# Kernel tuning notes

Hardware: AMD Instinct MI355X
Metric: run time of the kernel (lower is better)

The kernel has to match this reference:

```python
import jax, jax.numpy as jnp
import numpy as np

# (multiplicity, irrep_dim) for irreps_in == irreps_out: 128x0e + 64x1o + 32x2e
IRREPS = [(128, 1), (64, 3), (32, 5)]
NUM_INDICES = 64
N_ELEMENTS = 8192
SCALE = 1.0  # module's `scale` arg; total coeff = scale / sqrt(num_indices) / sqrt(mul_in)
W_DIM = sum(m * m for m, _ in IRREPS)  # 21504


def setup_inputs() -> dict:
    key = jax.random.key(0)
    ks = jax.random.split(key, 5)
    x0 = jax.random.normal(ks[0], (N_ELEMENTS, 128, 1), jnp.float32)
    x1 = jax.random.normal(ks[1], (N_ELEMENTS, 64, 3), jnp.float32)
    x2 = jax.random.normal(ks[2], (N_ELEMENTS, 32, 5), jnp.float32)
    w = jax.random.normal(ks[3], (NUM_INDICES, W_DIM), jnp.float32)
    # Random contiguous segment sizes that sum exactly to N_ELEMENTS:
    bnd = jnp.sort(jax.random.randint(ks[4], (NUM_INDICES - 1,), 0, N_ELEMENTS + 1)).astype(jnp.int32)
    counts = jnp.diff(jnp.concatenate([jnp.zeros((1,), jnp.int32), bnd,
                                       jnp.full((1,), N_ELEMENTS, jnp.int32)]))
    return {"x0": x0, "x1": x1, "x2": x2, "w": w, "num_index_counts": counts}


def reference(x0, x1, x2, w, num_index_counts):
    """Indexed (segmented) equivariant linear: rows are grouped contiguously by
    num_index_counts; segment g uses weight row w[g]. Per matched irrep the
    weight block is a (mul_in, mul_out) mixing matrix applied identically to
    each of the ir.dim components (Schur's lemma), with fan-in normalization
    1/sqrt(mul_in) (cue.descriptors.linear) times scale/sqrt(num_indices)."""
    n = x0.shape[0]
    # segment id per row (rows are already grouped contiguously, as in Repeats())
    sid = jnp.repeat(jnp.arange(NUM_INDICES), num_index_counts, total_repeat_length=n)
    xs = (x0, x1, x2)
    ys = []
    off = 0
    for xk, (mul, ir_dim) in zip(xs, IRREPS):
        blk = w[:, off:off + mul * mul].reshape(NUM_INDICES, mul, mul)  # (E, m_in, m_out)
        coeff = float(SCALE / np.sqrt(NUM_INDICES) / np.sqrt(mul))
        wk = blk[sid]  # (n, m_in, m_out) per-row weight gather
        # y[n, o, i] = coeff * sum_m x[n, m, i] * w[g(n), m, o]
        ys.append(coeff * jnp.einsum('nmi,nmo->noi', xk, wk))
        off += mul * mul
    return tuple(ys)
```

## Files before the change

### kernel.cpp

```cpp
#include <hip/hip_runtime.h>

typedef __attribute__((ext_vector_type(8))) short bf16x8;
typedef __attribute__((ext_vector_type(4))) float f32x4;

#define NSEG 64
#define NROW 8192
#define WROW 21504
#define NBPP 576
#define T0   64
#define T12  16
#define PA   136
#define PB   136
#define P1   196
#define P2   164

__device__ __forceinline__ unsigned short f2bf(float f) {
    unsigned u = __float_as_uint(f);
    u += 0x7fffu + ((u >> 16) & 1u);
    return (unsigned short)(u >> 16);
}

__global__ __launch_bounds__(256) void iil_kernel(
    const float* __restrict__ x0, const float* __restrict__ x1, const float* __restrict__ x2,
    const float* __restrict__ w, const int* __restrict__ counts,
    float* __restrict__ y0, float* __restrict__ y1, float* __restrict__ y2)
{
    __shared__ __align__(16) unsigned short smem_u[T0 * PA + 128 * PB];
    __shared__ int sstart[NSEG + 1];
    __shared__ int t16s[NSEG + 1];
    __shared__ int t64s[NSEG + 1];

    const int t = threadIdx.x;

    if (t < NSEG) {
        int c = counts[t];
        int v = c;
        #pragma unroll
        for (int d = 1; d < NSEG; d <<= 1) {
            int u = __shfl_up(v, d, 64);
            if (t >= d) v += u;
        }
        sstart[t + 1] = v;
        int a = (c + 15) >> 4;
        #pragma unroll
        for (int d = 1; d < NSEG; d <<= 1) {
            int u = __shfl_up(a, d, 64);
            if (t >= d) a += u;
        }
        t16s[t + 1] = a;
        int b2 = (c + 63) >> 6;
        #pragma unroll
        for (int d = 1; d < NSEG; d <<= 1) {
            int u = __shfl_up(b2, d, 64);
            if (t >= d) b2 += u;
        }
        t64s[t + 1] = b2;
        if (t == 0) { sstart[0] = 0; t16s[0] = 0; t64s[0] = 0; }
    }
    __syncthreads();

    const int phase = blockIdx.x / NBPP;
    const int pb = blockIdx.x - phase * NBPP;
    const float4 z4 = make_float4(0.f, 0.f, 0.f, 0.f);
    float* sbuf = (float*)smem_u;

    if (phase == 0) {
        if (pb >= t64s[NSEG]) return;
        int lo = 0, hi = NSEG;
        while (hi - lo > 1) {
            int mid = (lo + hi) >> 1;
            if (t64s[mid] <= pb) lo = mid; else hi = mid;
        }
        const int g = lo;
        const int s = sstart[g] + (pb - t64s[g]) * T0;
        const int nr = min(T0, sstart[g + 1] - s);
        const float* __restrict__ wseg = w + (size_t)g * WROW;

        unsigned short* As = smem_u;
        unsigned short* Bs = smem_u + T0 * PA;

        const float4* g0 = (const float4*)x0 + (size_t)s * 32;
        #pragma unroll
        for (int i = 0; i < 8; ++i) {
            int idx = t + i * 256;
            int r = idx >> 5, c4 = (idx & 31) * 4;
            float4 v = (r < nr) ? g0[idx] : z4;
            ushort4 bv;
            bv.x = f2bf(v.x); bv.y = f2bf(v.y); bv.z = f2bf(v.z); bv.w = f2bf(v.w);
            *(ushort4*)(As + r * PA + c4) = bv;
        }
        #pragma unroll
        for (int i = 0; i < 8; ++i) {
            int idx = t + i * 256;
            int k2 = idx >> 5;
            int o4 = (idx & 31) * 4;
            float4 va = *(const float4*)(wseg + (size_t)(2 * k2) * 128 + o4);
            float4 vb = *(const float4*)(wseg + (size_t)(2 * k2 + 1) * 128 + o4);
            *(ushort2*)(Bs + (size_t)(o4 + 0) * PB + 2 * k2) = make_ushort2(f2bf(va.x), f2bf(vb.x));
            *(ushort2*)(Bs + (size_t)(o4 + 1) * PB + 2 * k2) = make_ushort2(f2bf(va.y), f2bf(vb.y));
            *(ushort2*)(Bs + (size_t)(o4 + 2) * PB + 2 * k2) = make_ushort2(f2bf(va.z), f2bf(vb.z));
            *(ushort2*)(Bs + (size_t)(o4 + 3) * PB + 2 * k2) = make_ushort2(f2bf(va.w), f2bf(vb.w));
        }
        __syncthreads();

        const int lane = t & 63;
        const int wv = t >> 6;
        const int l16 = lane & 15;
        const int quad = lane >> 4;
        const int mp = wv & 1;
        const int np = wv >> 1;

        f32x4 acc[2][4];
        #pragma unroll
        for (int mt = 0; mt < 2; ++mt)
            #pragma unroll
            for (int nt = 0; nt < 4; ++nt)
                acc[mt][nt] = (f32x4){0.f, 0.f, 0.f, 0.f};

        const unsigned short* Abase = As + ((2 * mp) * 16 + l16) * PA + quad * 8;
        const unsigned short* Bbase = Bs + (size_t)((4 * np) * 16 + l16) * PB + quad * 8;

        #pragma unroll
        for (int ks = 0; ks < 4; ++ks) {
            const int ko = ks * 32;
            bf16x8 a0 = *(const bf16x8*)(Abase + ko);
            bf16x8 a1 = *(const bf16x8*)(Abase + 16 * PA + ko);
            #pragma unroll
            for (int nt = 0; nt < 4; ++nt) {
                bf16x8 b = *(const bf16x8*)(Bbase + (size_t)nt * 16 * PB + ko);
                acc[0][nt] = __builtin_amdgcn_mfma_f32_16x16x32_bf16(a0, b, acc[0][nt], 0, 0, 0);
                acc[1][nt] = __builtin_amdgcn_mfma_f32_16x16x32_bf16(a1, b, acc[1][nt], 0, 0, 0);
            }
        }

        const float c0 = 0.011048543456039806f;
        #pragma unroll
        for (int mt = 0; mt < 2; ++mt) {
            int rbase = (2 * mp + mt) * 16 + quad * 4;
            #pragma unroll
            for (int nt = 0; nt < 4; ++nt) {
                int col = (4 * np + nt) * 16 + l16;
                #pragma unroll
                for (int rg = 0; rg < 4; ++rg) {
                    int r = rbase + rg;
                    if (r < nr)
                        y0[(size_t)(s + r) * 128 + col] = acc[mt][nt][rg] * c0;
                }
            }
        }
    } else if (phase == 1) {
        if (pb >= t16s[NSEG]) return;
        int lo = 0, hi = NSEG;
        while (hi - lo > 1) {
            int mid = (lo + hi) >> 1;
            if (t16s[mid] <= pb) lo = mid; else hi = mid;
        }
        const int g = lo;
        const int s = sstart[g] + (pb - t16s[g]) * T12;
        const int nr = min(T12, sstart[g + 1] - s);
        const float* __restrict__ wseg = w + (size_t)g * WROW;

        float* sx1 = sbuf;
        const float4* g1 = (const float4*)x1 + (size_t)s * 48;
        #pragma unroll
        for (int i = 0; i < 3; ++i) {
            int idx = t + i * 256;
            int r = idx / 48, c = idx - r * 48;
            float4 v = (r < nr) ? g1[idx] : z4;
            *(float4*)(sx1 + r * P1 + c * 4) = v;
        }
        __syncthreads();

        const int og = t & 15;
        const int r = t >> 4;
        const float* xrow = sx1 + r * P1;
        const float* wp = wseg + 16384 + og * 4;
        float acc[12];
        #pragma unroll
        for (int i = 0; i < 12; ++i) acc[i] = 0.f;
        #pragma unroll 2
        for (int kq = 0; kq < 16; ++kq) {
            float4 xq0 = *(const float4*)(xrow + 12 * kq + 0);
            float4 xq1 = *(const float4*)(xrow + 12 * kq + 4);
            float4 xq2 = *(const float4*)(xrow + 12 * kq + 8);
            float xf[12] = {xq0.x, xq0.y, xq0.z, xq0.w,
                            xq1.x, xq1.y, xq1.z, xq1.w,
                            xq2.x, xq2.y, xq2.z, xq2.w};
            #pragma unroll
            for (int kk = 0; kk < 4; ++kk) {
                float4 wv = *(const float4*)(wp + (size_t)(4 * kq + kk) * 64);
                #pragma unroll
                for (int oo = 0; oo < 4; ++oo) {
                    float wvo = (oo == 0) ? wv.x : (oo == 1) ? wv.y : (oo == 2) ? wv.z : wv.w;
                    acc[oo * 3 + 0] = fmaf(wvo, xf[kk * 3 + 0], acc[oo * 3 + 0]);
                    acc[oo * 3 + 1] = fmaf(wvo, xf[kk * 3 + 1], acc[oo * 3 + 1]);
                    acc[oo * 3 + 2] = fmaf(wvo, xf[kk * 3 + 2], acc[oo * 3 + 2]);
                }
            }
        }
        const float c1 = 0.015625f;
        if (r < nr) {
            float* yb = y1 + (size_t)(s + r) * 192 + og * 12;
            *(float4*)(yb + 0) = make_float4(acc[0] * c1, acc[1] * c1, acc[2] * c1, acc[3] * c1);
            *(float4*)(yb + 4) = make_float4(acc[4] * c1, acc[5] * c1, acc[6] * c1, acc[7] * c1);
            *(float4*)(yb + 8) = make_float4(acc[8] * c1, acc[9] * c1, acc[10] * c1, acc[11] * c1);
        }
    } else {
        if (pb >= t16s[NSEG]) return;
        int lo = 0, hi = NSEG;
        while (hi - lo > 1) {
            int mid = (lo + hi) >> 1;
            if (t16s[mid] <= pb) lo = mid; else hi = mid;
        }
        const int g = lo;
        const int s = sstart[g] + (pb - t16s[g]) * T12;
        const int nr = min(T12, sstart[g + 1] - s);
        const float* __restrict__ wseg = w + (size_t)g * WROW;

        float* sx2 = sbuf;
        const float4* g2 = (const float4*)x2 + (size_t)s * 40;
        #pragma unroll
        for (int i = 0; i < 3; ++i) {
            int idx = t + i * 256;
            if (idx < 640) {
                int r = idx / 40, c = idx - r * 40;
                float4 v = (r < nr) ? g2[idx] : z4;
                *(float4*)(sx2 + r * P2 + c * 4) = v;
            }
        }
        __syncthreads();

        const int og = t & 15;
        const int r = t >> 4;
        const float* xrow = sx2 + r * P2;
        const float* wp = wseg + 20480 + og * 2;
        float acc[10];
        #pragma unroll
        for (int i = 0; i < 10; ++i) acc[i] = 0.f;
        #pragma unroll
        for (int kq = 0; kq < 8; ++kq) {
            float xf[20];
            #pragma unroll
            for (int j = 0; j < 5; ++j) {
                float4 v = *(const float4*)(xrow + 20 * kq + 4 * j);
                xf[4 * j + 0] = v.x; xf[4 * j + 1] = v.y; xf[4 * j + 2] = v.z; xf[4 * j + 3] = v.w;
            }
            #pragma unroll
            for (int kk = 0; kk < 4; ++kk) {
                float2 wv = *(const float2*)(wp + (size_t)(4 * kq + kk) * 32);
                #pragma unroll
                for (int i = 0; i < 5; ++i) {
                    acc[i]     = fmaf(wv.x, xf[5 * kk + i], acc[i]);
                    acc[5 + i] = fmaf(wv.y, xf[5 * kk + i], acc[5 + i]);
                }
            }
        }
        const float c2 = 0.022097086912079608f;
        if (r < nr) {
            float* yb = y2 + (size_t)(s + r) * 160 + og * 10;
            #pragma unroll
            for (int i = 0; i < 5; ++i)
                *(float2*)(yb + 2 * i) = make_float2(acc[2 * i] * c2, acc[2 * i + 1] * c2);
        }
    }
}

extern "C" void kernel_launch(void* const* d_in, const int* in_sizes, int n_in,
                              void* d_out, int out_size, void* d_ws, size_t ws_size,
                              hipStream_t stream) {
    const float* x0 = (const float*)d_in[0];
    const float* x1 = (const float*)d_in[1];
    const float* x2 = (const float*)d_in[2];
    const float* w  = (const float*)d_in[3];
    const int* counts = (const int*)d_in[4];

    float* y0 = (float*)d_out;
    float* y1 = y0 + (size_t)NROW * 128;
    float* y2 = y1 + (size_t)NROW * 192;

    hipLaunchKernelGGL(iil_kernel, dim3(3 * NBPP), dim3(256), 0, stream,
                       x0, x1, x2, w, counts, y0, y1, y2);
}
```

Before: 95.27 us.

## Precompute bf16 x0 and transposed bf16 weights in a prep kernel

Adds a prep kernel that converts x0 to bf16 and transposes and converts each segment's 128x128 weight block to bf16 in a workspace buffer. The phase-0 path of the main kernel then loads pre-converted A tiles and reads B fragments straight from global memory rather than staging them through shared memory. This removes repeated per-block weight conversion and transpose and halves x0 load bytes, at the cost of an extra launch and an extra round trip through global memory.

After: 99.05 us. +4.0%, slower.

```diff
diff --git a/kernel.cpp b/kernel.cpp
--- a/kernel.cpp
+++ b/kernel.cpp
@@ -10,7 +10,6 @@
 #define T0   64
 #define T12  16
 #define PA   136
-#define PB   136
 #define P1   196
 #define P2   164
 
@@ -20,12 +19,52 @@
     return (unsigned short)(u >> 16);
 }
 
+__global__ __launch_bounds__(256) void prep_kernel(
+    const float* __restrict__ x0, const float* __restrict__ w,
+    unsigned short* __restrict__ x0b, unsigned short* __restrict__ wt)
+{
+    const int t = threadIdx.x;
+    const int b = blockIdx.x;
+    if (b < 1024) {
+        int i = b * 256 + t;
+        float4 v = ((const float4*)x0)[i];
+        ushort4 o;
+        o.x = f2bf(v.x); o.y = f2bf(v.y); o.z = f2bf(v.z); o.w = f2bf(v.w);
+        *(ushort4*)(x0b + (size_t)i * 4) = o;
+    } else {
+        __shared__ float lw[128 * 132];
+        const int g = b - 1024;
+        const float* wseg = w + (size_t)g * WROW;
+        #pragma unroll
+        for (int i = 0; i < 16; ++i) {
+            int idx = t + i * 256;
+            int r = idx >> 5, c4 = (idx & 31) * 4;
+            float4 v = *(const float4*)(wseg + (size_t)r * 128 + c4);
+            *(float4*)(lw + r * 132 + c4) = v;
+        }
+        __syncthreads();
+        unsigned short* wo = wt + (size_t)g * 16384;
+        #pragma unroll
+        for (int i = 0; i < 16; ++i) {
+            int idx = t + i * 256;
+            int o = idx >> 5, k0 = (idx & 31) * 4;
+            ushort4 v;
+            v.x = f2bf(lw[(k0 + 0) * 132 + o]);
+            v.y = f2bf(lw[(k0 + 1) * 132 + o]);
+            v.z = f2bf(lw[(k0 + 2) * 132 + o]);
+            v.w = f2bf(lw[(k0 + 3) * 132 + o]);
+            *(ushort4*)(wo + (size_t)o * 128 + k0) = v;
+        }
+    }
+}
+
 __global__ __launch_bounds__(256) void iil_kernel(
-    const float* __restrict__ x0, const float* __restrict__ x1, const float* __restrict__ x2,
+    const float* __restrict__ x1, const float* __restrict__ x2,
     const float* __restrict__ w, const int* __restrict__ counts,
+    const unsigned short* __restrict__ x0b, const unsigned short* __restrict__ wt,
     float* __restrict__ y0, float* __restrict__ y1, float* __restrict__ y2)
 {
-    __shared__ __align__(16) unsigned short smem_u[T0 * PA + 128 * PB];
+    __shared__ __align__(16) unsigned short smem_u[T0 * PA];
     __shared__ int sstart[NSEG + 1];
     __shared__ int t16s[NSEG + 1];
     __shared__ int t64s[NSEG + 1];
@@ -74,32 +113,18 @@
         const int g = lo;
         const int s = sstart[g] + (pb - t64s[g]) * T0;
         const int nr = min(T0, sstart[g + 1] - s);
-        const float* __restrict__ wseg = w + (size_t)g * WROW;
 
         unsigned short* As = smem_u;
-        unsigned short* Bs = smem_u + T0 * PA;
-
-        const float4* g0 = (const float4*)x0 + (size_t)s * 32;
-        #pragma unroll
-        for (int i = 0; i < 8; ++i) {
-            int idx = t + i * 256;
-            int r = idx >> 5, c4 = (idx & 31) * 4;
-            float4 v = (r < nr) ? g0[idx] : z4;
-            ushort4 bv;
-            bv.x = f2bf(v.x); bv.y = f2bf(v.y); bv.z = f2bf(v.z); bv.w = f2bf(v.w);
-            *(ushort4*)(As + r * PA + c4) = bv;
-        }
-        #pragma unroll
-        for (int i = 0; i < 8; ++i) {
-            int idx = t + i * 256;
-            int k2 = idx >> 5;
-            int o4 = (idx & 31) * 4;
-            float4 va = *(const float4*)(wseg + (size_t)(2 * k2) * 128 + o4);
-            float4 vb = *(const float4*)(wseg + (size_t)(2 * k2 + 1) * 128 + o4);
-            *(ushort2*)(Bs + (size_t)(o4 + 0) * PB + 2 * k2) = make_ushort2(f2bf(va.x), f2bf(vb.x));
-            *(ushort2*)(Bs + (size_t)(o4 + 1) * PB + 2 * k2) = make_ushort2(f2bf(va.y), f2bf(vb.y));
-            *(ushort2*)(Bs + (size_t)(o4 + 2) * PB + 2 * k2) = make_ushort2(f2bf(va.z), f2bf(vb.z));
-            *(ushort2*)(Bs + (size_t)(o4 + 3) * PB + 2 * k2) = make_ushort2(f2bf(va.w), f2bf(vb.w));
+        {
+            const uint4* src = (const uint4*)(x0b + (size_t)s * 128);
+            const uint4 zz = make_uint4(0u, 0u, 0u, 0u);
+            #pragma unroll
+            for (int i = 0; i < 4; ++i) {
+                int idx = t + i * 256;
+                int r = idx >> 4, c8 = idx & 15;
+                uint4 v = (r < nr) ? src[idx] : zz;
+                *(uint4*)(As + r * PA + c8 * 8) = v;
+            }
         }
         __syncthreads();
 
@@ -118,7 +143,8 @@
                 acc[mt][nt] = (f32x4){0.f, 0.f, 0.f, 0.f};
 
         const unsigned short* Abase = As + ((2 * mp) * 16 + l16) * PA + quad * 8;
-        const unsigned short* Bbase = Bs + (size_t)((4 * np) * 16 + l16) * PB + quad * 8;
+        const unsigned short* Bbase = wt + (size_t)g * 16384
+                                    + (size_t)((4 * np) * 16 + l16) * 128 + quad * 8;
 
         #pragma unroll
         for (int ks = 0; ks < 4; ++ks) {
@@ -127,9 +153,9 @@
             bf16x8 a1 = *(const bf16x8*)(Abase + 16 * PA + ko);
             #pragma unroll
             for (int nt = 0; nt < 4; ++nt) {
-                bf16x8 b = *(const bf16x8*)(Bbase + (size_t)nt * 16 * PB + ko);
-                acc[0][nt] = __builtin_amdgcn_mfma_f32_16x16x32_bf16(a0, b, acc[0][nt], 0, 0, 0);
-                acc[1][nt] = __builtin_amdgcn_mfma_f32_16x16x32_bf16(a1, b, acc[1][nt], 0, 0, 0);
+                bf16x8 bfr = *(const bf16x8*)(Bbase + (size_t)nt * 16 * 128 + ko);
+                acc[0][nt] = __builtin_amdgcn_mfma_f32_16x16x32_bf16(a0, bfr, acc[0][nt], 0, 0, 0);
+                acc[1][nt] = __builtin_amdgcn_mfma_f32_16x16x32_bf16(a1, bfr, acc[1][nt], 0, 0, 0);
             }
         }
 
@@ -278,6 +304,11 @@
     float* y1 = y0 + (size_t)NROW * 128;
     float* y2 = y1 + (size_t)NROW * 192;
 
+    unsigned short* x0b = (unsigned short*)d_ws;
+    unsigned short* wtp = x0b + (size_t)NROW * 128;
+
+    hipLaunchKernelGGL(prep_kernel, dim3(1024 + NSEG), dim3(256), 0, stream,
+                       x0, w, x0b, wtp);
     hipLaunchKernelGGL(iil_kernel, dim3(3 * NBPP), dim3(256), 0, stream,
-                       x0, x1, x2, w, counts, y0, y1, y2);
+                       x1, x2, w, counts, x0b, wtp, y0, y1, y2);
 }
```
